# Kernel optimization log

Measured on AMD Instinct MI355X. Metric: run time of the kernel, lower is better.

Reference implementation:

```python
import jax, jax.numpy as jnp
import numpy as np

B, S, VOCAB, P, K, R = 64, 512, 50000, 300, 50, 5


def setup_inputs() -> dict:
    key = jax.random.key(0)
    k0, k1, k2, k3, k4, k5, k6 = jax.random.split(key, 7)
    idx = jax.random.randint(k0, (B, S), 0, VOCAB)
    emb = jax.random.normal(k1, (VOCAB, P), dtype=jnp.float32) * 0.02
    emb = emb.at[0].set(0.0)  # padding_idx=0 row is zero
    C = jax.random.normal(k2, (K, P), dtype=jnp.float32)  # label embeddings ~ N(0,1)
    conv_w = jax.random.normal(k3, (1, 1, 1, 2 * R + 1), dtype=jnp.float32) * 0.1
    conv_b = jax.random.normal(k4, (1,), dtype=jnp.float32) * 0.1
    W2 = jax.random.normal(k5, (K, P), dtype=jnp.float32) / np.sqrt(P).astype(np.float32)
    b2 = jax.random.normal(k6, (K,), dtype=jnp.float32) * 0.01
    return {"idx": idx, "emb": emb, "C": C, "conv_w": conv_w, "conv_b": conv_b, "W2": W2, "b2": b2}


def reference(idx, emb, C, conv_w, conv_b, W2, b2):
    # Embed sentence: [B, S, P]
    x = emb[idx]
    # Cosine label attention
    x_hat = x / (jnp.linalg.norm(x, axis=2, keepdims=True) + 0.001)
    l_hat = C / (jnp.linalg.norm(C, axis=1, keepdims=True) + 0.001)
    G_hat = jnp.einsum('kp,bsp->bks', l_hat, x_hat)  # [B, K, S]
    # Pad seq dim by R on both sides, then conv2d(1->1, kernel (1, 2R+1))
    G_pad = jnp.pad(G_hat, ((0, 0), (0, 0), (R, R)))
    m = jax.lax.conv_general_dilated(
        G_pad[:, None, :, :], conv_w, window_strides=(1, 1), padding='VALID',
        dimension_numbers=('NCHW', 'OIHW', 'NCHW'))[:, 0] + conv_b[0]  # [B, K, S]
    m = jax.nn.relu(m)
    m = jnp.max(m, axis=1)  # max over labels -> [B, S]
    beta = jax.nn.softmax(m, axis=1)[..., None]  # [B, S, 1]
    pooled = jnp.mean(beta * x, axis=1)  # [B, P]
    # Dropout is identity in eval mode; final linear P -> K
    return pooled @ W2.T + b2
```

## Files before the change

kernel.cpp:

```cpp
#include <hip/hip_runtime.h>

#define B_   64
#define S_   512
#define P_   300
#define K_   50
#define MPAD 64
#define LDX  344
#define LDG  528

typedef short short8v __attribute__((ext_vector_type(8)));
typedef float float4v __attribute__((ext_vector_type(4)));

__device__ __forceinline__ short f2bf(float f) {
  unsigned u = __builtin_bit_cast(unsigned, f);
  u = (u + 0x7FFFu + ((u >> 16) & 1u)) >> 16;
  return (short)u;
}
__device__ __forceinline__ float bf2f(short h) {
  return __builtin_bit_cast(float, ((unsigned)(unsigned short)h) << 16);
}

__global__ __launch_bounds__(64) void k1_prep(const float* __restrict__ C,
                                              const float* __restrict__ W2,
                                              short* __restrict__ apack) {
  int bid = blockIdx.x;
  int mat = bid / 40;
  int rem = bid - mat * 40;
  int mt  = rem / 10;
  int ks  = rem - mt * 10;
  int lane = threadIdx.x;
  __shared__ float invn[16];
  if (mat == 0) {
    int rl = lane >> 2, q = lane & 3;
    int m = mt * 16 + rl;
    float ss = 0.f;
    if (m < K_) {
      for (int p = q; p < P_; p += 4) { float v = C[m * P_ + p]; ss += v * v; }
    }
    ss += __shfl_xor(ss, 1);
    ss += __shfl_xor(ss, 2);
    if (q == 0) invn[rl] = 1.f / (sqrtf(ss) + 0.001f);
  }
  __syncthreads();
  int ml = lane & 15, quad = lane >> 4;
  int m = mt * 16 + ml;
  const float* src = (mat == 0) ? C : W2;
  short8v v8;
  #pragma unroll
  for (int j = 0; j < 8; ++j) {
    int k = ks * 32 + quad * 8 + j;
    float v = 0.f;
    if (m < K_ && k < P_) {
      v = src[m * P_ + k];
      if (mat == 0) v *= invn[ml];
    }
    v8[j] = f2bf(v);
  }
  *(short8v*)(apack + (size_t)(((mat * 4 + mt) * 10 + ks) * 512 + lane * 8)) = v8;
}

__global__ __launch_bounds__(256) void k2_gemm(const int* __restrict__ idx,
                                               const float* __restrict__ emb,
                                               const short* __restrict__ apack,
                                               short* __restrict__ G,
                                               short* __restrict__ Yt) {
  __shared__ __align__(16) short xt[64][LDX];
  __shared__ float scale_s[64];
  int bid = blockIdx.x;
  int b = bid >> 3, s0 = (bid & 7) * 64;
  int tid = threadIdx.x;
  int w = tid >> 6, lane = tid & 63;

  float ssr[16];
  #pragma unroll
  for (int r = 0; r < 16; ++r) {
    int ls = w * 16 + r;
    int row = idx[b * S_ + s0 + ls];
    const float4* src = (const float4*)(emb + (size_t)row * P_);
    float4 v = src[lane];
    float ss = v.x * v.x + v.y * v.y + v.z * v.z + v.w * v.w;
    short4 h; h.x = f2bf(v.x); h.y = f2bf(v.y); h.z = f2bf(v.z); h.w = f2bf(v.w);
    *(short4*)&xt[ls][4 * lane] = h;
    if (lane < 11) {
      float4 v2 = src[64 + lane];
      ss += v2.x * v2.x + v2.y * v2.y + v2.z * v2.z + v2.w * v2.w;
      short4 h2; h2.x = f2bf(v2.x); h2.y = f2bf(v2.y); h2.z = f2bf(v2.z); h2.w = f2bf(v2.w);
      *(short4*)&xt[ls][256 + 4 * lane] = h2;
    } else if (lane < 16) {
      short4 z = {0, 0, 0, 0};
      *(short4*)&xt[ls][300 + 4 * (lane - 11)] = z;
    }
    ssr[r] = ss;
  }
  #pragma unroll
  for (int r = 0; r < 16; ++r) {
    float ss = ssr[r];
    #pragma unroll
    for (int off = 32; off > 0; off >>= 1) ss += __shfl_xor(ss, off);
    if (lane == 0) scale_s[w * 16 + r] = 1.f / (sqrtf(ss) + 0.001f);
  }
  __syncthreads();

  float4v accG[4] = {}, accY[4] = {};
  int ml = lane & 15, quad = lane >> 4;
  const short8v* a1p = (const short8v*)(apack) + (size_t)((0 * 4 + w) * 10) * 64 + lane;
  const short8v* a2p = (const short8v*)(apack) + (size_t)((1 * 4 + w) * 10) * 64 + lane;
  #pragma unroll
  for (int ks = 0; ks < 10; ++ks) {
    short8v a1 = a1p[ks * 64];
    short8v a2 = a2p[ks * 64];
    int kk = ks * 32 + quad * 8;
    #pragma unroll
    for (int nt = 0; nt < 4; ++nt) {
      short8v bf = *(const short8v*)&xt[nt * 16 + ml][kk];
      accG[nt] = __builtin_amdgcn_mfma_f32_16x16x32_bf16(a1, bf, accG[nt], 0, 0, 0);
      accY[nt] = __builtin_amdgcn_mfma_f32_16x16x32_bf16(a2, bf, accY[nt], 0, 0, 0);
    }
  }

  #pragma unroll
  for (int nt = 0; nt < 4; ++nt) {
    int sl = nt * 16 + ml;
    float sc = scale_s[sl];
    int sg = s0 + sl;
    #pragma unroll
    for (int reg = 0; reg < 4; ++reg) {
      int m = w * 16 + quad * 4 + reg;
      if (m < K_) {
        G [(size_t)(b * MPAD + m) * S_ + sg] = f2bf(accG[nt][reg] * sc);
        Yt[(size_t)(b * MPAD + m) * S_ + sg] = f2bf(accY[nt][reg]);
      }
    }
  }
}

__global__ __launch_bounds__(512) void k3_fused(const short* __restrict__ G,
                                                const float* __restrict__ conv_w,
                                                const float* __restrict__ conv_b,
                                                const short* __restrict__ Yt,
                                                const float* __restrict__ b2,
                                                float* __restrict__ out) {
  __shared__ __align__(16) float gt[K_][LDG];
  __shared__ float beta[S_];
  __shared__ float red[8];
  int b = blockIdx.x;
  int tid = threadIdx.x;
  int lane = tid & 63, wv = tid >> 6;

  for (int e = tid; e < K_ * 8; e += 512) {
    int k = e >> 3, j = e & 7;
    gt[k][j] = 0.f;
    gt[k][520 + j] = 0.f;
  }
  for (int k = wv; k < K_; k += 8) {
    short8v v = *(const short8v*)(G + (((size_t)(b * MPAD + k)) << 9) + lane * 8);
    float* dst = &gt[k][8 + lane * 8];
    float4 f0, f1;
    f0.x = bf2f(v[0]); f0.y = bf2f(v[1]); f0.z = bf2f(v[2]); f0.w = bf2f(v[3]);
    f1.x = bf2f(v[4]); f1.y = bf2f(v[5]); f1.z = bf2f(v[6]); f1.w = bf2f(v[7]);
    *(float4*)dst = f0;
    *(float4*)(dst + 4) = f1;
  }
  float wvv[11];
  #pragma unroll
  for (int t = 0; t < 11; ++t) wvv[t] = conv_w[t];
  float cb = conv_b[0];
  __syncthreads();

  float mx = 0.f;
  for (int k = 0; k < K_; ++k) {
    float acc = cb;
    #pragma unroll
    for (int t = 0; t < 11; ++t) acc += wvv[t] * gt[k][3 + tid + t];
    mx = fmaxf(mx, fmaxf(acc, 0.f));
  }

  float r = mx;
  #pragma unroll
  for (int off = 32; off > 0; off >>= 1) r = fmaxf(r, __shfl_xor(r, off));
  if (lane == 0) red[wv] = r;
  __syncthreads();
  float bm = red[0];
  #pragma unroll
  for (int i = 1; i < 8; ++i) bm = fmaxf(bm, red[i]);
  float e = __expf(mx - bm);
  r = e;
  #pragma unroll
  for (int off = 32; off > 0; off >>= 1) r += __shfl_xor(r, off);
  __syncthreads();
  if (lane == 0) red[wv] = r;
  __syncthreads();
  float sum = 0.f;
  #pragma unroll
  for (int i = 0; i < 8; ++i) sum += red[i];
  beta[tid] = e / (sum * (float)S_);
  __syncthreads();

  for (int k = wv; k < K_; k += 8) {
    short8v y = *(const short8v*)(Yt + (((size_t)(b * MPAD + k)) << 9) + lane * 8);
    const float4* bp = (const float4*)&beta[lane * 8];
    float4 b0 = bp[0], b1 = bp[1];
    float acc = b0.x * bf2f(y[0]) + b0.y * bf2f(y[1]) +
                b0.z * bf2f(y[2]) + b0.w * bf2f(y[3]) +
                b1.x * bf2f(y[4]) + b1.y * bf2f(y[5]) +
                b1.z * bf2f(y[6]) + b1.w * bf2f(y[7]);
    #pragma unroll
    for (int off = 32; off > 0; off >>= 1) acc += __shfl_xor(acc, off);
    if (lane == 0) out[b * K_ + k] = acc + b2[k];
  }
}

extern "C" void kernel_launch(void* const* d_in, const int* in_sizes, int n_in,
                              void* d_out, int out_size, void* d_ws, size_t ws_size,
                              hipStream_t stream) {
  const int*   idx    = (const int*)  d_in[0];
  const float* emb    = (const float*)d_in[1];
  const float* C      = (const float*)d_in[2];
  const float* conv_w = (const float*)d_in[3];
  const float* conv_b = (const float*)d_in[4];
  const float* W2     = (const float*)d_in[5];
  const float* b2     = (const float*)d_in[6];
  float* out = (float*)d_out;

  char* ws = (char*)d_ws;
  short* apack = (short*)(ws);
  short* G     = (short*)(ws + 81920);
  short* Yt    = (short*)(ws + 81920 + 4194304);

  hipLaunchKernelGGL(k1_prep,  dim3(80),  dim3(64),  0, stream, C, W2, apack);
  hipLaunchKernelGGL(k2_gemm,  dim3(512), dim3(256), 0, stream, idx, emb, apack, G, Yt);
  hipLaunchKernelGGL(k3_fused, dim3(64),  dim3(512), 0, stream, G, conv_w, conv_b, Yt, b2, out);
}
```

Measured before the change: 157.8 us.

## Fuse conv and label-max into GEMM kernel using halo rows

The GEMM kernel now loads 80 sequence rows per block (64 plus an 8-row halo on each side), computes G for all of them, and runs the 11-tap convolution, ReLU and max over labels in shared memory. It writes only a per-position max (mbuf) instead of the full bf16 G tensor. The pooling kernel then just does the softmax and the weighted sum over Yt. This removes the G write and read round trip and the large shared-memory staging in the final kernel, at the cost of about 25% extra gather and MFMA work on halo rows and an added synchronisation inside the GEMM kernel.

```diff
diff --git a/kernel.cpp b/kernel.cpp
--- a/kernel.cpp
+++ b/kernel.cpp
@@ -6,7 +6,8 @@
 #define K_   50
 #define MPAD 64
 #define LDX  344
-#define LDG  528
+#define NS   80
+#define LDGS 81
 
 typedef short short8v __attribute__((ext_vector_type(8)));
 typedef float float4v __attribute__((ext_vector_type(4)));
@@ -62,46 +63,62 @@
 __global__ __launch_bounds__(256) void k2_gemm(const int* __restrict__ idx,
                                                const float* __restrict__ emb,
                                                const short* __restrict__ apack,
-                                               short* __restrict__ G,
-                                               short* __restrict__ Yt) {
-  __shared__ __align__(16) short xt[64][LDX];
-  __shared__ float scale_s[64];
+                                               short* __restrict__ Yt,
+                                               const float* __restrict__ conv_w,
+                                               const float* __restrict__ conv_b,
+                                               float* __restrict__ mbuf) {
+  __shared__ __align__(16) char smem_raw[NS * LDX * 2];
+  __shared__ float scale_s[NS];
+  __shared__ float mpart[4][64];
+  short (*xt)[LDX]  = (short(*)[LDX])smem_raw;
+  float (*gs)[LDGS] = (float(*)[LDGS])smem_raw;
+
   int bid = blockIdx.x;
   int b = bid >> 3, s0 = (bid & 7) * 64;
   int tid = threadIdx.x;
   int w = tid >> 6, lane = tid & 63;
 
-  float ssr[16];
-  #pragma unroll
-  for (int r = 0; r < 16; ++r) {
-    int ls = w * 16 + r;
-    int row = idx[b * S_ + s0 + ls];
-    const float4* src = (const float4*)(emb + (size_t)row * P_);
-    float4 v = src[lane];
-    float ss = v.x * v.x + v.y * v.y + v.z * v.z + v.w * v.w;
-    short4 h; h.x = f2bf(v.x); h.y = f2bf(v.y); h.z = f2bf(v.z); h.w = f2bf(v.w);
-    *(short4*)&xt[ls][4 * lane] = h;
-    if (lane < 11) {
-      float4 v2 = src[64 + lane];
-      ss += v2.x * v2.x + v2.y * v2.y + v2.z * v2.z + v2.w * v2.w;
-      short4 h2; h2.x = f2bf(v2.x); h2.y = f2bf(v2.y); h2.z = f2bf(v2.z); h2.w = f2bf(v2.w);
-      *(short4*)&xt[ls][256 + 4 * lane] = h2;
-    } else if (lane < 16) {
+  float ssr[20];
+  #pragma unroll
+  for (int r = 0; r < 20; ++r) {
+    int ls = w * 20 + r;
+    int sg = s0 - 8 + ls;
+    float ss = 0.f;
+    if (sg >= 0 && sg < S_) {
+      int row = idx[b * S_ + sg];
+      const float4* src = (const float4*)(emb + (size_t)row * P_);
+      float4 v = src[lane];
+      ss = v.x * v.x + v.y * v.y + v.z * v.z + v.w * v.w;
+      short4 h; h.x = f2bf(v.x); h.y = f2bf(v.y); h.z = f2bf(v.z); h.w = f2bf(v.w);
+      *(short4*)&xt[ls][4 * lane] = h;
+      if (lane < 11) {
+        float4 v2 = src[64 + lane];
+        ss += v2.x * v2.x + v2.y * v2.y + v2.z * v2.z + v2.w * v2.w;
+        short4 h2; h2.x = f2bf(v2.x); h2.y = f2bf(v2.y); h2.z = f2bf(v2.z); h2.w = f2bf(v2.w);
+        *(short4*)&xt[ls][256 + 4 * lane] = h2;
+      } else if (lane < 16) {
+        short4 z = {0, 0, 0, 0};
+        *(short4*)&xt[ls][300 + 4 * (lane - 11)] = z;
+      }
+    } else {
       short4 z = {0, 0, 0, 0};
-      *(short4*)&xt[ls][300 + 4 * (lane - 11)] = z;
+      *(short4*)&xt[ls][4 * lane] = z;
+      if (lane < 11)       *(short4*)&xt[ls][256 + 4 * lane] = z;
+      else if (lane < 16)  *(short4*)&xt[ls][300 + 4 * (lane - 11)] = z;
     }
     ssr[r] = ss;
   }
   #pragma unroll
-  for (int r = 0; r < 16; ++r) {
+  for (int r = 0; r < 20; ++r) {
     float ss = ssr[r];
     #pragma unroll
     for (int off = 32; off > 0; off >>= 1) ss += __shfl_xor(ss, off);
-    if (lane == 0) scale_s[w * 16 + r] = 1.f / (sqrtf(ss) + 0.001f);
-  }
-  __syncthreads();
-
-  float4v accG[4] = {}, accY[4] = {};
+    if (lane == 0) scale_s[w * 20 + r] = 1.f / (sqrtf(ss) + 0.001f);
+  }
+  __syncthreads();
+
+  float4v accG[5] = {};
+  float4v accY[4] = {};
   int ml = lane & 15, quad = lane >> 4;
   const short8v* a1p = (const short8v*)(apack) + (size_t)((0 * 4 + w) * 10) * 64 + lane;
   const short8v* a2p = (const short8v*)(apack) + (size_t)((1 * 4 + w) * 10) * 64 + lane;
@@ -111,69 +128,73 @@
     short8v a2 = a2p[ks * 64];
     int kk = ks * 32 + quad * 8;
     #pragma unroll
+    for (int nt = 0; nt < 5; ++nt) {
+      short8v bg = *(const short8v*)&xt[nt * 16 + ml][kk];
+      accG[nt] = __builtin_amdgcn_mfma_f32_16x16x32_bf16(a1, bg, accG[nt], 0, 0, 0);
+    }
+    #pragma unroll
     for (int nt = 0; nt < 4; ++nt) {
-      short8v bf = *(const short8v*)&xt[nt * 16 + ml][kk];
-      accG[nt] = __builtin_amdgcn_mfma_f32_16x16x32_bf16(a1, bf, accG[nt], 0, 0, 0);
-      accY[nt] = __builtin_amdgcn_mfma_f32_16x16x32_bf16(a2, bf, accY[nt], 0, 0, 0);
+      short8v by = *(const short8v*)&xt[8 + nt * 16 + ml][kk];
+      accY[nt] = __builtin_amdgcn_mfma_f32_16x16x32_bf16(a2, by, accY[nt], 0, 0, 0);
     }
   }
 
   #pragma unroll
   for (int nt = 0; nt < 4; ++nt) {
-    int sl = nt * 16 + ml;
-    float sc = scale_s[sl];
-    int sg = s0 + sl;
+    int sg = s0 + nt * 16 + ml;
     #pragma unroll
     for (int reg = 0; reg < 4; ++reg) {
       int m = w * 16 + quad * 4 + reg;
-      if (m < K_) {
-        G [(size_t)(b * MPAD + m) * S_ + sg] = f2bf(accG[nt][reg] * sc);
-        Yt[(size_t)(b * MPAD + m) * S_ + sg] = f2bf(accY[nt][reg]);
-      }
-    }
-  }
-}
-
-__global__ __launch_bounds__(512) void k3_fused(const short* __restrict__ G,
-                                                const float* __restrict__ conv_w,
-                                                const float* __restrict__ conv_b,
-                                                const short* __restrict__ Yt,
-                                                const float* __restrict__ b2,
-                                                float* __restrict__ out) {
-  __shared__ __align__(16) float gt[K_][LDG];
+      if (m < K_) Yt[(size_t)(b * MPAD + m) * S_ + sg] = f2bf(accY[nt][reg]);
+    }
+  }
+
+  float wvv[11];
+  #pragma unroll
+  for (int t = 0; t < 11; ++t) wvv[t] = conv_w[t];
+  float cb = conv_b[0];
+
+  __syncthreads();
+
+  #pragma unroll
+  for (int nt = 0; nt < 5; ++nt) {
+    int scol = nt * 16 + ml;
+    float sc = scale_s[scol];
+    #pragma unroll
+    for (int reg = 0; reg < 4; ++reg) {
+      int m = w * 16 + quad * 4 + reg;
+      gs[m][scol] = accG[nt][reg] * sc;
+    }
+  }
+  __syncthreads();
+
+  float part = 0.f;
+  for (int k = w; k < K_; k += 4) {
+    float acc = cb;
+    #pragma unroll
+    for (int t = 0; t < 11; ++t) acc += wvv[t] * gs[k][lane + 3 + t];
+    part = fmaxf(part, fmaxf(acc, 0.f));
+  }
+  mpart[w][lane] = part;
+  __syncthreads();
+  if (tid < 64) {
+    float m0 = fmaxf(fmaxf(mpart[0][tid], mpart[1][tid]),
+                     fmaxf(mpart[2][tid], mpart[3][tid]));
+    mbuf[b * S_ + s0 + tid] = m0;
+  }
+}
+
+__global__ __launch_bounds__(512) void k3_pool(const float* __restrict__ mbuf,
+                                               const short* __restrict__ Yt,
+                                               const float* __restrict__ b2,
+                                               float* __restrict__ out) {
   __shared__ float beta[S_];
   __shared__ float red[8];
   int b = blockIdx.x;
   int tid = threadIdx.x;
   int lane = tid & 63, wv = tid >> 6;
 
-  for (int e = tid; e < K_ * 8; e += 512) {
-    int k = e >> 3, j = e & 7;
-    gt[k][j] = 0.f;
-    gt[k][520 + j] = 0.f;
-  }
-  for (int k = wv; k < K_; k += 8) {
-    short8v v = *(const short8v*)(G + (((size_t)(b * MPAD + k)) << 9) + lane * 8);
-    float* dst = &gt[k][8 + lane * 8];
-    float4 f0, f1;
-    f0.x = bf2f(v[0]); f0.y = bf2f(v[1]); f0.z = bf2f(v[2]); f0.w = bf2f(v[3]);
-    f1.x = bf2f(v[4]); f1.y = bf2f(v[5]); f1.z = bf2f(v[6]); f1.w = bf2f(v[7]);
-    *(float4*)dst = f0;
-    *(float4*)(dst + 4) = f1;
-  }
-  float wvv[11];
-  #pragma unroll
-  for (int t = 0; t < 11; ++t) wvv[t] = conv_w[t];
-  float cb = conv_b[0];
-  __syncthreads();
-
-  float mx = 0.f;
-  for (int k = 0; k < K_; ++k) {
-    float acc = cb;
-    #pragma unroll
-    for (int t = 0; t < 11; ++t) acc += wvv[t] * gt[k][3 + tid + t];
-    mx = fmaxf(mx, fmaxf(acc, 0.f));
-  }
+  float mx = mbuf[b * S_ + tid];
 
   float r = mx;
   #pragma unroll
@@ -224,10 +245,11 @@
 
   char* ws = (char*)d_ws;
   short* apack = (short*)(ws);
-  short* G     = (short*)(ws + 81920);
-  short* Yt    = (short*)(ws + 81920 + 4194304);
-
-  hipLaunchKernelGGL(k1_prep,  dim3(80),  dim3(64),  0, stream, C, W2, apack);
-  hipLaunchKernelGGL(k2_gemm,  dim3(512), dim3(256), 0, stream, idx, emb, apack, G, Yt);
-  hipLaunchKernelGGL(k3_fused, dim3(64),  dim3(512), 0, stream, G, conv_w, conv_b, Yt, b2, out);
-}
+  short* Yt    = (short*)(ws + 81920);
+  float* mbuf  = (float*)(ws + 81920 + 4194304);
+
+  hipLaunchKernelGGL(k1_prep, dim3(80),  dim3(64),  0, stream, C, W2, apack);
+  hipLaunchKernelGGL(k2_gemm, dim3(512), dim3(256), 0, stream,
+                     idx, emb, apack, Yt, conv_w, conv_b, mbuf);
+  hipLaunchKernelGGL(k3_pool, dim3(64),  dim3(512), 0, stream, mbuf, Yt, b2, out);
+}
```

Measured after the change: 157.8 us. Within noise of the previous version (-0.0%).
